# Kernel optimization log

Measured on AMD Instinct MI355X. Metric: run time of the kernel, lower is better.

The kernel has to match this reference:

```python
import jax, jax.numpy as jnp
import numpy as np

B, S, H, K = 8, 2048, 768, 128
FILTERS = (1, 3, 5)
C = H // len(FILTERS)  # 256 channels per conv, concat -> H
LN_EPS = 1e-05
COS_EPS = 1e-08


def setup_inputs() -> dict:
    key = jax.random.key(0)
    ks = jax.random.split(key, 16)
    mk = lambda k, shape: jax.random.normal(k, shape, dtype=jnp.float32) * 0.02
    return {
        "representation": jax.random.normal(ks[0], (B, S, H), dtype=jnp.float32),
        "src_mask": jnp.ones((B, S), dtype=jnp.float32),
        # conv weights stored as [k, H_in, C_out] for lax 1D conv (torch Conv2d(1,C,(k,H)))
        "enc_conv_w1": mk(ks[1], (1, H, C)),
        "enc_conv_w3": mk(ks[2], (3, H, C)),
        "enc_conv_w5": mk(ks[3], (5, H, C)),
        "ln_g": jnp.ones((H,), jnp.float32),
        "ln_b": jnp.zeros((H,), jnp.float32),
        "enc_lin_w": mk(ks[4], (H, H)),   # torch Linear weight [out,in]
        "enc_tr_w": mk(ks[5], (K, H)),
        "dec_tr_w": mk(ks[6], (H, K)),
        "dec_conv_w1": mk(ks[7], (1, H, C)),
        "dec_conv_w3": mk(ks[8], (3, H, C)),
        "dec_conv_w5": mk(ks[9], (5, H, C)),
        "dec_lin_w": mk(ks[10], (H, H)),
        "out_lin_w": mk(ks[11], (H, H)),
    }


def _multi_conv(x, ws):
    # x: [B, S, H]; each w: [k, H, C]; torch pads (k//2, 0) -> same-length for odd k
    outs = []
    for w in ws:
        k = w.shape[0]
        outs.append(jax.lax.conv_general_dilated(
            x, w, window_strides=(1,), padding=[(k // 2, k // 2)],
            dimension_numbers=("NWC", "WIO", "NWC")))
    return jnp.concatenate(outs, axis=-1)  # [B, S, H]


def _layernorm(x, g, b):
    mu = jnp.mean(x, axis=-1, keepdims=True)
    var = jnp.mean((x - mu) ** 2, axis=-1, keepdims=True)
    return (x - mu) * jax.lax.rsqrt(var + LN_EPS) * g + b


def reference(representation, src_mask, enc_conv_w1, enc_conv_w3, enc_conv_w5,
              ln_g, ln_b, enc_lin_w, enc_tr_w, dec_tr_w,
              dec_conv_w1, dec_conv_w3, dec_conv_w5, dec_lin_w, out_lin_w):
    # ---- AutoEncoder (dropout layers are identity in eval mode) ----
    h = _multi_conv(representation, (enc_conv_w1, enc_conv_w3, enc_conv_w5))
    h = _layernorm(h + representation, ln_g, ln_b)
    h = jnp.tanh(h @ enc_lin_w.T)
    location = h @ enc_tr_w.T            # [B, S, K] (encode_out)
    d = location @ dec_tr_w.T            # [B, S, H]
    d = _multi_conv(d, (dec_conv_w1, dec_conv_w3, dec_conv_w5))
    d = jnp.tanh(d @ dec_lin_w.T)
    decode_out = d @ out_lin_w.T         # [B, S, H]

    # ---- banded pairwise cosine similarity (fuses the torch shift loop) ----
    # torch loop writes dis_matrix[b, i, i+s+1] = cos(loc[b, i+s+1], loc[b, i])
    # for s in range(max_act_len), i.e. the strict upper band of the symmetric
    # pairwise cosine-similarity matrix with offsets 1..max_act_len.
    normed = location / jnp.maximum(
        jnp.sqrt(jnp.sum(location * location, axis=-1, keepdims=True)), COS_EPS)
    sim = jnp.einsum("bid,bjd->bij", normed, normed)  # [B, S, S]
    offs = jnp.arange(S)[None, :] - jnp.arange(S)[:, None]  # j - i
    max_act_len = jnp.max(jnp.sum(src_mask, axis=-1)).astype(jnp.int32)
    band = (offs >= 1) & (offs <= max_act_len)        # [S, S]
    dis_matrix = jnp.where(band[None], sim, 0.0)
    src_dis_mask = src_mask[:, :, None] * src_mask[:, None, :]
    act_dis_tags = band[None].astype(jnp.float32) * src_dis_mask
    return (location, dis_matrix, act_dis_tags, decode_out)
```

## Files before the change

### kernel.cpp

```cpp
#include <hip/hip_runtime.h>

#define B_   8
#define S_   2048
#define H_   768
#define K_   128
#define C_   256
#define SH_  2052
#define MTOK (B_*S_)

typedef __attribute__((ext_vector_type(8))) short short8;
typedef __attribute__((ext_vector_type(4))) float f32x4;

typedef __attribute__((address_space(1))) const void gvoid;
typedef __attribute__((address_space(3))) void lvoid;

__device__ __forceinline__ void gload16(const void* g, void* l) {
    __builtin_amdgcn_global_load_lds((gvoid*)g, (lvoid*)l, 16, 0, 0);
}

__device__ __forceinline__ ushort f2b(float f) {
    union { float f; unsigned u; } v; v.f = f;
    unsigned r = v.u + 0x7fffu + ((v.u >> 16) & 1u);
    return (ushort)(r >> 16);
}
__device__ __forceinline__ float b2f(ushort u) {
    union { unsigned u; float f; } v; v.u = ((unsigned)u) << 16;
    return v.f;
}
__device__ __forceinline__ float fast_tanh(float x) {
    float e = __expf(2.f * x);
    return 1.f - 2.f / (e + 1.f);
}


__global__ __launch_bounds__(512) void k_maxlen(const float* __restrict__ mask, int* Lp) {
    __shared__ float sh[8];
    const int tid = threadIdx.x;
    float mx = 0.f;
    for (int b = 0; b < B_; ++b) {
        const float4 v = ((const float4*)(mask + b * S_))[tid];
        float s = v.x + v.y + v.z + v.w;
#pragma unroll
        for (int off = 32; off; off >>= 1) s += __shfl_xor(s, off);
        if ((tid & 63) == 0) sh[tid >> 6] = s;
        __syncthreads();
        if (tid == 0) {
            float t = 0.f;
#pragma unroll
            for (int q = 0; q < 8; ++q) t += sh[q];
            mx = fmaxf(mx, t);
        }
        __syncthreads();
    }
    if (tid == 0) *Lp = (int)mx;
}

__global__ void k_build_xh(const float* __restrict__ rep, ushort* __restrict__ xh) {
    int i = blockIdx.x * blockDim.x + threadIdx.x;
    const int stride = gridDim.x * blockDim.x;
    const int n4 = B_ * SH_ * H_ / 4;
    for (; i < n4; i += stride) {
        const int idx = i * 4;
        const int h = idx % H_;
        const int rs = idx / H_;
        const int s = rs % SH_;
        const int b = rs / SH_;
        ushort4 o; o.x = 0; o.y = 0; o.z = 0; o.w = 0;
        if (s >= 2 && s < S_ + 2) {
            const float4 v = *(const float4*)(rep + ((size_t)b * S_ + (s - 2)) * H_ + h);
            o.x = f2b(v.x); o.y = f2b(v.y); o.z = f2b(v.z); o.w = f2b(v.w);
        }
        *(ushort4*)(xh + idx) = o;
    }
}

struct CvtE { const float* src; ushort* dst; int n; int kh; };
struct CvtAll { CvtE e[11]; };

__global__ void k_cvt_all(CvtAll a) {
    const CvtE e = a.e[blockIdx.y];
    int i = blockIdx.x * blockDim.x + threadIdx.x;
    const int stride = gridDim.x * blockDim.x;
    for (; i < e.n; i += stride) {
        if (e.kh) {
            const int c = i / e.kh;
            const int r = i - c * e.kh;
            e.dst[i] = f2b(e.src[r * C_ + c]);
        } else {
            e.dst[i] = f2b(e.src[i]);
        }
    }
}


struct G3P {
    const ushort* A;
    const ushort* W0;
    const ushort* W1;
    const ushort* W2;
    int Ktot;
    int lda;
    ushort* outB; int ldoB;
    float*  outF; int ldoF;
    int act;
    int nMtiles;
};

template<bool CONV>
__global__ __launch_bounds__(512, 2) void g3(G3P p) {
    constexpr int ASEG = 1024;
    constexpr int BSEG = 2048;
    constexpr int BUFE = (ASEG + BSEG) * 8;
    __shared__ __align__(16) ushort lds[3][BUFE];

    const int tid = threadIdx.x;
    const int w = tid >> 6, lane = tid & 63;
    const int l15 = lane & 15, lk = lane >> 4;
    const int wr = w >> 2, wc = w & 3;
    const int axor = l15 & 7;

    int m_base, n_base, nt, Ktot, arow0;
    const ushort* Wt;
    if (CONV) {
        const int nM = p.nMtiles;
        int idx = blockIdx.x;
        int br;
        if (idx < nM) br = 2;
        else if (idx < 2 * nM) { br = 1; idx -= nM; }
        else { br = 0; idx -= 2 * nM; }
        m_base = idx * 128;
        n_base = br * 256;
        nt = 12 * (2 * br + 1);
        Ktot = 768 * (2 * br + 1);
        Wt = (br == 0) ? p.W0 : (br == 1) ? p.W1 : p.W2;
        arow0 = m_base + ((m_base >> 11) << 2) + (2 - br);
    } else {
        m_base = blockIdx.x * 128;
        n_base = blockIdx.y * 256;
        nt = p.Ktot >> 6;
        Ktot = p.Ktot;
        Wt = p.W0;
        arow0 = m_base;
    }

    auto stage1 = [&](int kt, int bufi, int q) {
        const int kk = kt << 6;
        int rowoff = 0, h0 = kk;
        if (CONV) { const int tap = kt / 12; rowoff = tap; h0 = (kt - tap * 12) << 6; }
        if (q < 2) {
            const int seg = q * 512 + tid;
            const int row = seg >> 3;
            const int slot = (seg & 7) ^ (row & 7);
            gload16(p.A + (size_t)(arow0 + rowoff + row) * p.lda + h0 + slot * 8,
                    &lds[bufi][seg * 8]);
        } else {
            const int seg = (q - 2) * 512 + tid;
            const int row = seg >> 3;
            const int slot = (seg & 7) ^ (row & 7);
            const int wrow = (CONV ? 0 : n_base) + row;
            gload16(Wt + (size_t)wrow * Ktot + kk + slot * 8,
                    &lds[bufi][ASEG * 8 + seg * 8]);
        }
    };
    auto stage = [&](int kt, int bufi) {
#pragma unroll
        for (int q = 0; q < 6; ++q) stage1(kt, bufi, q);
    };

    f32x4 acc[4][4] = {};

    stage(0, 0);
    stage(1, 1);

    int buf = 0;
    for (int t = 0; t < nt; ++t) {
        const ushort* Ab = &lds[buf][0];
        const ushort* Bb = &lds[buf][ASEG * 8];
        if (t + 1 < nt) asm volatile("s_waitcnt vmcnt(6)" ::: "memory");
        else            asm volatile("s_waitcnt vmcnt(0)" ::: "memory");
        __builtin_amdgcn_sched_barrier(0);
        asm volatile("s_barrier" ::: "memory");
        __builtin_amdgcn_sched_barrier(0);

        int nbuf = buf + 2; if (nbuf >= 3) nbuf -= 3;
        const bool sb = (t + 2 < nt);

#pragma unroll
        for (int ks = 0; ks < 2; ++ks) {
            short8 bq[4], aq[4];
#pragma unroll
            for (int ni = 0; ni < 4; ++ni)
                bq[ni] = *(const short8*)(Bb + (wc * 64 + ni * 16 + l15) * 64 + ((((ks << 2) | lk) ^ axor) << 3));
#pragma unroll
            for (int mi = 0; mi < 4; ++mi)
                aq[mi] = *(const short8*)(Ab + (wr * 64 + mi * 16 + l15) * 64 + ((((ks << 2) | lk) ^ axor) << 3));
            if (sb) { stage1(t + 2, nbuf, 3 * ks); stage1(t + 2, nbuf, 3 * ks + 1); stage1(t + 2, nbuf, 3 * ks + 2); }
            asm volatile("s_waitcnt lgkmcnt(0)" ::: "memory");
            __builtin_amdgcn_sched_barrier(0);
            __builtin_amdgcn_s_setprio(1);
#pragma unroll
            for (int mi = 0; mi < 4; ++mi)
#pragma unroll
                for (int ni = 0; ni < 4; ++ni)
                    acc[mi][ni] = __builtin_amdgcn_mfma_f32_16x16x32_bf16(aq[mi], bq[ni], acc[mi][ni], 0, 0, 0);
            __builtin_amdgcn_s_setprio(0);
            __builtin_amdgcn_sched_barrier(0);
        }
        ++buf; if (buf == 3) buf = 0;
    }

#pragma unroll
    for (int mi = 0; mi < 4; ++mi)
#pragma unroll
        for (int ni = 0; ni < 4; ++ni)
#pragma unroll
            for (int jj = 0; jj < 4; ++jj) {
                const int r = m_base + wr * 64 + mi * 16 + 4 * lk + jj;
                const int n = n_base + wc * 64 + ni * 16 + l15;
                float v = acc[mi][ni][jj];
                if (p.act) v = fast_tanh(v);
                if (p.outF) p.outF[(size_t)r * p.ldoF + n] = v;
                if (p.outB) p.outB[(size_t)r * p.ldoB + n] = f2b(v);
            }
}


struct GemmP {
    const ushort* A;
    const ushort* Wt;
    int Ktot;
    int lda;
    ushort* outB;
    int ldoB;
    int outB_halo;
    float* outF;
    int ldoF;
    int act;
};

template<int BM, int BN>
__global__ __launch_bounds__(256) void gemm_lds(GemmP p) {
    constexpr int MF = BM / 32;
    constexpr int NF = BN / 32;
    __shared__ __align__(16) ushort As[BM * 64];
    __shared__ __align__(16) ushort Bs[BN * 64];
    const int tid = threadIdx.x;
    const int w = tid >> 6, lane = tid & 63;
    const int l15 = lane & 15, lk = lane >> 4;
    const int m_base = blockIdx.x * BM;
    const int n_base = blockIdx.y * BN;
    const int wr = w >> 1, wc = w & 1;
    f32x4 acc[MF][NF] = {};
    const int srow = lane >> 3;
    const int scol = (lane & 7) * 8;
    const int nk = p.Ktot >> 6;

    for (int kt = 0; kt < nk; ++kt) {
        const int kk = kt << 6;
#pragma unroll
        for (int q = 0; q < BM / 32; ++q) {
            const int r = w * (BM / 4) + q * 8;
            gload16(p.A + (size_t)(m_base + r + srow) * p.lda + kk + scol, As + r * 64);
        }
#pragma unroll
        for (int q = 0; q < BN / 32; ++q) {
            const int r = w * (BN / 4) + q * 8;
            gload16(p.Wt + (size_t)(n_base + r + srow) * p.Ktot + kk + scol, Bs + r * 64);
        }
        __syncthreads();
#pragma unroll
        for (int ks = 0; ks < 2; ++ks) {
            short8 af[MF], bfr[NF];
#pragma unroll
            for (int i = 0; i < MF; ++i)
                af[i] = *(const short8*)(As + (wr * (BM / 2) + i * 16 + l15) * 64 + ks * 32 + 8 * lk);
#pragma unroll
            for (int j = 0; j < NF; ++j)
                bfr[j] = *(const short8*)(Bs + (wc * (BN / 2) + j * 16 + l15) * 64 + ks * 32 + 8 * lk);
#pragma unroll
            for (int i = 0; i < MF; ++i)
#pragma unroll
                for (int j = 0; j < NF; ++j)
                    acc[i][j] = __builtin_amdgcn_mfma_f32_16x16x32_bf16(af[i], bfr[j], acc[i][j], 0, 0, 0);
        }
        __syncthreads();
    }

    const int bb4 = ((m_base >> 11) << 2) + 2;
#pragma unroll
    for (int i = 0; i < MF; ++i)
#pragma unroll
        for (int j = 0; j < NF; ++j)
#pragma unroll
            for (int jj = 0; jj < 4; ++jj) {
                const int r = m_base + wr * (BM / 2) + i * 16 + 4 * lk + jj;
                const int n = n_base + wc * (BN / 2) + j * 16 + l15;
                float v = acc[i][j][jj];
                if (p.act) v = fast_tanh(v);
                if (p.outF) p.outF[(size_t)r * p.ldoF + n] = v;
                if (p.outB) {
                    const int rr = p.outB_halo ? (r + bb4) : r;
                    p.outB[(size_t)rr * p.ldoB + n] = f2b(v);
                }
            }
}


__global__ __launch_bounds__(192) void k_ln(const ushort* __restrict__ conv,
                                            const float* __restrict__ rep,
                                            const float* __restrict__ gw,
                                            const float* __restrict__ bw,
                                            ushort* __restrict__ out) {
    const int row = blockIdx.x;
    const int tid = threadIdx.x;
    const int h = tid * 4;
    const ushort4 cv = *(const ushort4*)(conv + (size_t)row * H_ + h);
    const float4  rv = *(const float4*)(rep + (size_t)row * H_ + h);
    float v[4] = { b2f(cv.x) + rv.x, b2f(cv.y) + rv.y, b2f(cv.z) + rv.z, b2f(cv.w) + rv.w };
    float s1 = v[0] + v[1] + v[2] + v[3];
    float s2 = v[0]*v[0] + v[1]*v[1] + v[2]*v[2] + v[3]*v[3];
#pragma unroll
    for (int off = 32; off; off >>= 1) { s1 += __shfl_xor(s1, off); s2 += __shfl_xor(s2, off); }
    __shared__ float sh[6];
    const int wid = tid >> 6, lane = tid & 63;
    if (lane == 0) { sh[wid] = s1; sh[3 + wid] = s2; }
    __syncthreads();
    s1 = sh[0] + sh[1] + sh[2];
    s2 = sh[3] + sh[4] + sh[5];
    const float mu  = s1 * (1.f / H_);
    const float var = s2 * (1.f / H_) - mu * mu;
    const float rs  = rsqrtf(var + 1e-5f);
    const float4 gv = *(const float4*)(gw + h);
    const float4 bv = *(const float4*)(bw + h);
    ushort4 o;
    o.x = f2b((v[0] - mu) * rs * gv.x + bv.x);
    o.y = f2b((v[1] - mu) * rs * gv.y + bv.y);
    o.z = f2b((v[2] - mu) * rs * gv.z + bv.z);
    o.w = f2b((v[3] - mu) * rs * gv.w + bv.w);
    *(ushort4*)(out + (size_t)row * H_ + h) = o;
}


__global__ __launch_bounds__(256) void k_normed(const float* __restrict__ loc, ushort* __restrict__ out) {
    const int wid = threadIdx.x >> 6, lane = threadIdx.x & 63;
    const int row = blockIdx.x * 4 + wid;
    const float* lp = loc + (size_t)row * K_;
    const float x0 = lp[lane], x1 = lp[lane + 64];
    float ss = x0 * x0 + x1 * x1;
#pragma unroll
    for (int off = 32; off; off >>= 1) ss += __shfl_xor(ss, off);
    const float sc = 1.f / fmaxf(sqrtf(ss), 1e-8f);
    ushort* op = out + (size_t)row * K_;
    op[lane] = f2b(x0 * sc);
    op[lane + 64] = f2b(x1 * sc);
}


__global__ __launch_bounds__(256) void k_simtags(const ushort* __restrict__ normed,
                                                 const float* __restrict__ mask,
                                                 const int* __restrict__ Lp,
                                                 float* __restrict__ dis,
                                                 float* __restrict__ tags) {
    const int wid = threadIdx.x >> 6, lane = threadIdx.x & 63;
    const int l15 = lane & 15, lk = lane >> 4;
    const int b   = blockIdx.z;
    const int i0b = blockIdx.x * 64;
    const int i0  = i0b + wid * 16;
    const int j0  = blockIdx.y * 64;
    const int L   = *Lp;
    f32x4 acc[4] = {};
    if ((j0 + 63 >= i0b + 1) && (j0 <= i0b + 63 + L)) {
        const ushort* nb = normed + (size_t)b * S_ * K_;
#pragma unroll
        for (int kt = 0; kt < 4; ++kt) {
            const int kk = kt * 32;
            const short8 a = *(const short8*)(nb + (size_t)(i0 + l15) * K_ + kk + 8 * lk);
#pragma unroll
            for (int j = 0; j < 4; ++j) {
                const short8 bfr = *(const short8*)(nb + (size_t)(j0 + j * 16 + l15) * K_ + kk + 8 * lk);
                acc[j] = __builtin_amdgcn_mfma_f32_16x16x32_bf16(a, bfr, acc[j], 0, 0, 0);
            }
        }
    }
    const float* mb = mask + b * S_;
    float* dp = dis  + (size_t)b * S_ * S_;
    float* tp = tags + (size_t)b * S_ * S_;
#pragma unroll
    for (int j = 0; j < 4; ++j) {
#pragma unroll
        for (int jj = 0; jj < 4; ++jj) {
            const int i  = i0 + 4 * lk + jj;
            const int jc = j0 + j * 16 + l15;
            const int d  = jc - i;
            const bool band = (d >= 1 && d <= L);
            dp[(size_t)i * S_ + jc] = band ? acc[j][jj] : 0.f;
            tp[(size_t)i * S_ + jc] = band ? mb[i] * mb[jc] : 0.f;
        }
    }
}


extern "C" void kernel_launch(void* const* d_in, const int* in_sizes, int n_in,
                              void* d_out, int out_size, void* d_ws, size_t ws_size,
                              hipStream_t stream) {
    const float* rep  = (const float*)d_in[0];
    const float* mask = (const float*)d_in[1];
    const float* ew1  = (const float*)d_in[2];
    const float* ew3  = (const float*)d_in[3];
    const float* ew5  = (const float*)d_in[4];
    const float* lng  = (const float*)d_in[5];
    const float* lnb  = (const float*)d_in[6];
    const float* elin = (const float*)d_in[7];
    const float* etr  = (const float*)d_in[8];
    const float* dtr  = (const float*)d_in[9];
    const float* dw1  = (const float*)d_in[10];
    const float* dw3  = (const float*)d_in[11];
    const float* dw5  = (const float*)d_in[12];
    const float* dlin = (const float*)d_in[13];
    const float* olin = (const float*)d_in[14];

    float* out_loc = (float*)d_out;
    float* out_dis = out_loc + (size_t)B_ * S_ * K_;
    float* out_tag = out_dis + (size_t)B_ * S_ * S_;
    float* out_dec = out_tag + (size_t)B_ * S_ * S_;

    char* ws = (char*)d_ws;
    size_t off = 0;
    auto alloc = [&](size_t bytes) -> char* {
        char* p = ws + off;
        off += (bytes + 255) & ~(size_t)255;
        return p;
    };
    int*    Lp    = (int*)alloc(256);
    ushort* Xh    = (ushort*)alloc((size_t)B_ * SH_ * H_ * 2);
    ushort* wte1  = (ushort*)alloc((size_t)C_ * 768 * 2);
    ushort* wte3  = (ushort*)alloc((size_t)C_ * 2304 * 2);
    ushort* wte5  = (ushort*)alloc((size_t)C_ * 3840 * 2);
    ushort* wtd1  = (ushort*)alloc((size_t)C_ * 768 * 2);
    ushort* wtd3  = (ushort*)alloc((size_t)C_ * 2304 * 2);
    ushort* wtd5  = (ushort*)alloc((size_t)C_ * 3840 * 2);
    ushort* welin = (ushort*)alloc((size_t)H_ * H_ * 2);
    ushort* wetr  = (ushort*)alloc((size_t)K_ * H_ * 2);
    ushort* wdtr  = (ushort*)alloc((size_t)H_ * K_ * 2);
    ushort* wdlin = (ushort*)alloc((size_t)H_ * H_ * 2);
    ushort* wolin = (ushort*)alloc((size_t)H_ * H_ * 2);
    ushort* bufB  = (ushort*)alloc((size_t)MTOK * H_ * 2);
    ushort* bufC  = (ushort*)alloc((size_t)MTOK * H_ * 2);
    ushort* bufD  = (ushort*)alloc((size_t)MTOK * H_ * 2);
    ushort* bufL  = (ushort*)alloc((size_t)MTOK * K_ * 2);
    ushort* bufN  = (ushort*)alloc((size_t)MTOK * K_ * 2);
    if (ws_size < off) return;

    k_maxlen<<<1, 512, 0, stream>>>(mask, Lp);
    k_build_xh<<<2048, 256, 0, stream>>>(rep, Xh);

    CvtAll ca;
    ca.e[0]  = { ew1,  wte1, 768 * C_,  768 };
    ca.e[1]  = { ew3,  wte3, 2304 * C_, 2304 };
    ca.e[2]  = { ew5,  wte5, 3840 * C_, 3840 };
    ca.e[3]  = { dw1,  wtd1, 768 * C_,  768 };
    ca.e[4]  = { dw3,  wtd3, 2304 * C_, 2304 };
    ca.e[5]  = { dw5,  wtd5, 3840 * C_, 3840 };
    ca.e[6]  = { elin, welin, H_ * H_, 0 };
    ca.e[7]  = { etr,  wetr,  K_ * H_, 0 };
    ca.e[8]  = { dtr,  wdtr,  H_ * K_, 0 };
    ca.e[9]  = { dlin, wdlin, H_ * H_, 0 };
    ca.e[10] = { olin, wolin, H_ * H_, 0 };
    k_cvt_all<<<dim3(256, 11), 256, 0, stream>>>(ca);

    {
        G3P p{}; p.A = Xh; p.W0 = wte1; p.W1 = wte3; p.W2 = wte5;
        p.lda = H_; p.outB = bufB; p.ldoB = H_; p.nMtiles = MTOK / 128;
        g3<true><<<3 * (MTOK / 128), 512, 0, stream>>>(p);
    }
    k_ln<<<MTOK, 192, 0, stream>>>(bufB, rep, lng, lnb, bufC);
    {
        G3P p{}; p.A = bufC; p.W0 = welin; p.Ktot = H_; p.lda = H_;
        p.outB = bufD; p.ldoB = H_; p.act = 1;
        g3<false><<<dim3(MTOK / 128, H_ / 256), 512, 0, stream>>>(p);
    }
    {
        GemmP p{}; p.A = bufD; p.lda = H_; p.Wt = wetr; p.Ktot = H_;
        p.outF = out_loc; p.ldoF = K_; p.outB = bufL; p.ldoB = K_;
        gemm_lds<64, 128><<<dim3(MTOK / 64, 1), 256, 0, stream>>>(p);
    }
    k_normed<<<MTOK / 4, 256, 0, stream>>>(out_loc, bufN);
    {
        GemmP p{}; p.A = bufL; p.lda = K_; p.Wt = wdtr; p.Ktot = K_;
        p.outB = Xh; p.ldoB = H_; p.outB_halo = 1;
        gemm_lds<128, 128><<<dim3(MTOK / 128, H_ / 128), 256, 0, stream>>>(p);
    }
    {
        G3P p{}; p.A = Xh; p.W0 = wtd1; p.W1 = wtd3; p.W2 = wtd5;
        p.lda = H_; p.outB = bufB; p.ldoB = H_; p.nMtiles = MTOK / 128;
        g3<true><<<3 * (MTOK / 128), 512, 0, stream>>>(p);
    }
    {
        G3P p{}; p.A = bufB; p.W0 = wdlin; p.Ktot = H_; p.lda = H_;
        p.outB = bufC; p.ldoB = H_; p.act = 1;
        g3<false><<<dim3(MTOK / 128, H_ / 256), 512, 0, stream>>>(p);
    }
    {
        G3P p{}; p.A = bufC; p.W0 = wolin; p.Ktot = H_; p.lda = H_;
        p.outF = out_dec; p.ldoF = H_;
        g3<false><<<dim3(MTOK / 128, H_ / 256), 512, 0, stream>>>(p);
    }
    k_simtags<<<dim3(S_ / 64, S_ / 64, B_), 256, 0, stream>>>(bufN, mask, Lp, out_dis, out_tag);
}
```

Baseline: 447.7 us.

## Use 256x256 tiles and split-K the 5-tap conv for balanced blocks

Replaces the 128x256 triple-buffered GEMM with a 256x256 double-buffered kernel that loads the A fragments in two halves, which raises reuse per LDS load. The conv grid is reorganised into four equal-work sets of 256 blocks by splitting the 5-tap branch's K into two partial sums held in fp32. The LayerNorm, or a new merge kernel on the decoder side, adds those partials. This aims to balance conv block durations and cut global traffic per FLOP, at the cost of extra fp32 partial-buffer traffic, one more kernel launch, and lower occupancy from larger tiles.

Measured after the change: 486.8 us. +8.7%, slower.

```diff
diff --git a/kernel.cpp b/kernel.cpp
--- a/kernel.cpp
+++ b/kernel.cpp
@@ -93,25 +93,22 @@
 }
 
 
-struct G3P {
+struct GBP {
     const ushort* A;
-    const ushort* W0;
-    const ushort* W1;
-    const ushort* W2;
+    const ushort* W;
+    const ushort* w1; const ushort* w3; const ushort* w5;
     int Ktot;
     int lda;
     ushort* outB; int ldoB;
     float*  outF; int ldoF;
     int act;
-    int nMtiles;
+    ushort* convB;
+    float* PA; float* PB;
 };
 
 template<bool CONV>
-__global__ __launch_bounds__(512, 2) void g3(G3P p) {
-    constexpr int ASEG = 1024;
-    constexpr int BSEG = 2048;
-    constexpr int BUFE = (ASEG + BSEG) * 8;
-    __shared__ __align__(16) ushort lds[3][BUFE];
+__global__ __launch_bounds__(512) void gemm_big(GBP p) {
+    __shared__ __align__(16) ushort lds[2][4096 * 8];
 
     const int tid = threadIdx.x;
     const int w = tid >> 6, lane = tid & 63;
@@ -119,108 +116,127 @@
     const int wr = w >> 2, wc = w & 3;
     const int axor = l15 & 7;
 
-    int m_base, n_base, nt, Ktot, arow0;
+    int m_base, n_base = 0, nt, kbase = 0, abase = 0, set = 0, wstride, lda = p.lda;
     const ushort* Wt;
     if (CONV) {
-        const int nM = p.nMtiles;
-        int idx = blockIdx.x;
-        int br;
-        if (idx < nM) br = 2;
-        else if (idx < 2 * nM) { br = 1; idx -= nM; }
-        else { br = 0; idx -= 2 * nM; }
-        m_base = idx * 128;
-        n_base = br * 256;
-        nt = 12 * (2 * br + 1);
-        Ktot = 768 * (2 * br + 1);
-        Wt = (br == 0) ? p.W0 : (br == 1) ? p.W1 : p.W2;
-        arow0 = m_base + ((m_base >> 11) << 2) + (2 - br);
+        set = blockIdx.x >> 6;
+        m_base = (blockIdx.x & 63) * 256;
+        if (set == 0)      { Wt = p.w5; wstride = 3840; kbase = 0;    abase = 0; nt = 36; }
+        else if (set == 1) { Wt = p.w3; wstride = 2304; kbase = 0;    abase = 1; nt = 36; }
+        else if (set == 2) { Wt = p.w5; wstride = 3840; kbase = 2304; abase = 3; nt = 24; }
+        else               { Wt = p.w1; wstride = 768;  kbase = 0;    abase = 2; nt = 12; }
     } else {
-        m_base = blockIdx.x * 128;
+        m_base = blockIdx.x * 256;
         n_base = blockIdx.y * 256;
-        nt = p.Ktot >> 6;
-        Ktot = p.Ktot;
-        Wt = p.W0;
-        arow0 = m_base;
-    }
-
-    auto stage1 = [&](int kt, int bufi, int q) {
-        const int kk = kt << 6;
-        int rowoff = 0, h0 = kk;
-        if (CONV) { const int tap = kt / 12; rowoff = tap; h0 = (kt - tap * 12) << 6; }
-        if (q < 2) {
+        Wt = p.W; wstride = p.Ktot; nt = p.Ktot >> 6;
+    }
+    const int bb = m_base >> 11;
+    const int arow0 = CONV ? (m_base + 4 * bb + abase) : m_base;
+
+    auto stage = [&](int kt, int bufi) {
+        int klocal = kt, taprow = 0;
+        if (CONV) { taprow = kt / 12; klocal = kt - taprow * 12; }
+        const int h0 = klocal << 6;
+        const int wcol = kbase + (kt << 6);
+        ushort* Ab = &lds[bufi][0];
+        ushort* Bb = &lds[bufi][2048 * 8];
+#pragma unroll
+        for (int q = 0; q < 4; ++q) {
             const int seg = q * 512 + tid;
             const int row = seg >> 3;
-            const int slot = (seg & 7) ^ (row & 7);
-            gload16(p.A + (size_t)(arow0 + rowoff + row) * p.lda + h0 + slot * 8,
-                    &lds[bufi][seg * 8]);
-        } else {
-            const int seg = (q - 2) * 512 + tid;
+            const int s = (seg & 7) ^ (row & 7);
+            gload16(p.A + (size_t)(arow0 + taprow + row) * lda + h0 + s * 8, Ab + seg * 8);
+        }
+#pragma unroll
+        for (int q = 0; q < 4; ++q) {
+            const int seg = q * 512 + tid;
             const int row = seg >> 3;
-            const int slot = (seg & 7) ^ (row & 7);
+            const int s = (seg & 7) ^ (row & 7);
             const int wrow = (CONV ? 0 : n_base) + row;
-            gload16(Wt + (size_t)wrow * Ktot + kk + slot * 8,
-                    &lds[bufi][ASEG * 8 + seg * 8]);
+            gload16(Wt + (size_t)wrow * wstride + wcol + s * 8, Bb + seg * 8);
         }
     };
-    auto stage = [&](int kt, int bufi) {
-#pragma unroll
-        for (int q = 0; q < 6; ++q) stage1(kt, bufi, q);
-    };
-
-    f32x4 acc[4][4] = {};
+
+    f32x4 acc[8][4] = {};
 
     stage(0, 0);
     stage(1, 1);
 
-    int buf = 0;
     for (int t = 0; t < nt; ++t) {
-        const ushort* Ab = &lds[buf][0];
-        const ushort* Bb = &lds[buf][ASEG * 8];
-        if (t + 1 < nt) asm volatile("s_waitcnt vmcnt(6)" ::: "memory");
+        const int cur = t & 1;
+        const ushort* Ab = &lds[cur][0];
+        const ushort* Bb = &lds[cur][2048 * 8];
+        if (t + 1 < nt) asm volatile("s_waitcnt vmcnt(8)" ::: "memory");
         else            asm volatile("s_waitcnt vmcnt(0)" ::: "memory");
         __builtin_amdgcn_sched_barrier(0);
         asm volatile("s_barrier" ::: "memory");
         __builtin_amdgcn_sched_barrier(0);
 
-        int nbuf = buf + 2; if (nbuf >= 3) nbuf -= 3;
-        const bool sb = (t + 2 < nt);
-
-#pragma unroll
-        for (int ks = 0; ks < 2; ++ks) {
-            short8 bq[4], aq[4];
-#pragma unroll
-            for (int ni = 0; ni < 4; ++ni)
-                bq[ni] = *(const short8*)(Bb + (wc * 64 + ni * 16 + l15) * 64 + ((((ks << 2) | lk) ^ axor) << 3));
-#pragma unroll
-            for (int mi = 0; mi < 4; ++mi)
-                aq[mi] = *(const short8*)(Ab + (wr * 64 + mi * 16 + l15) * 64 + ((((ks << 2) | lk) ^ axor) << 3));
-            if (sb) { stage1(t + 2, nbuf, 3 * ks); stage1(t + 2, nbuf, 3 * ks + 1); stage1(t + 2, nbuf, 3 * ks + 2); }
-            asm volatile("s_waitcnt lgkmcnt(0)" ::: "memory");
-            __builtin_amdgcn_sched_barrier(0);
-            __builtin_amdgcn_s_setprio(1);
-#pragma unroll
-            for (int mi = 0; mi < 4; ++mi)
-#pragma unroll
-                for (int ni = 0; ni < 4; ++ni)
-                    acc[mi][ni] = __builtin_amdgcn_mfma_f32_16x16x32_bf16(aq[mi], bq[ni], acc[mi][ni], 0, 0, 0);
-            __builtin_amdgcn_s_setprio(0);
-            __builtin_amdgcn_sched_barrier(0);
-        }
-        ++buf; if (buf == 3) buf = 0;
-    }
-
-#pragma unroll
-    for (int mi = 0; mi < 4; ++mi)
+        short8 af[4][2], bf[4][2];
+#pragma unroll
+        for (int mi = 0; mi < 4; ++mi)
+#pragma unroll
+            for (int ks = 0; ks < 2; ++ks)
+                af[mi][ks] = *(const short8*)(Ab + (wr * 128 + mi * 16 + l15) * 64 + ((((ks << 2) | lk) ^ axor) << 3));
 #pragma unroll
         for (int ni = 0; ni < 4; ++ni)
 #pragma unroll
+            for (int ks = 0; ks < 2; ++ks)
+                bf[ni][ks] = *(const short8*)(Bb + (wc * 64 + ni * 16 + l15) * 64 + ((((ks << 2) | lk) ^ axor) << 3));
+        asm volatile("s_waitcnt lgkmcnt(0)" ::: "memory");
+        __builtin_amdgcn_sched_barrier(0);
+        __builtin_amdgcn_s_setprio(1);
+#pragma unroll
+        for (int mi = 0; mi < 4; ++mi)
+#pragma unroll
+            for (int ni = 0; ni < 4; ++ni) {
+                acc[mi][ni] = __builtin_amdgcn_mfma_f32_16x16x32_bf16(af[mi][0], bf[ni][0], acc[mi][ni], 0, 0, 0);
+                acc[mi][ni] = __builtin_amdgcn_mfma_f32_16x16x32_bf16(af[mi][1], bf[ni][1], acc[mi][ni], 0, 0, 0);
+            }
+        __builtin_amdgcn_s_setprio(0);
+        __builtin_amdgcn_sched_barrier(0);
+#pragma unroll
+        for (int mi = 0; mi < 4; ++mi)
+#pragma unroll
+            for (int ks = 0; ks < 2; ++ks)
+                af[mi][ks] = *(const short8*)(Ab + (wr * 128 + (4 + mi) * 16 + l15) * 64 + ((((ks << 2) | lk) ^ axor) << 3));
+        asm volatile("s_waitcnt lgkmcnt(0)" ::: "memory");
+        __builtin_amdgcn_sched_barrier(0);
+        asm volatile("s_barrier" ::: "memory");
+        __builtin_amdgcn_sched_barrier(0);
+        if (t + 2 < nt) stage(t + 2, cur);
+        __builtin_amdgcn_sched_barrier(0);
+        __builtin_amdgcn_s_setprio(1);
+#pragma unroll
+        for (int mi = 0; mi < 4; ++mi)
+#pragma unroll
+            for (int ni = 0; ni < 4; ++ni) {
+                acc[4 + mi][ni] = __builtin_amdgcn_mfma_f32_16x16x32_bf16(af[mi][0], bf[ni][0], acc[4 + mi][ni], 0, 0, 0);
+                acc[4 + mi][ni] = __builtin_amdgcn_mfma_f32_16x16x32_bf16(af[mi][1], bf[ni][1], acc[4 + mi][ni], 0, 0, 0);
+            }
+        __builtin_amdgcn_s_setprio(0);
+        __builtin_amdgcn_sched_barrier(0);
+    }
+
+#pragma unroll
+    for (int fi = 0; fi < 8; ++fi)
+#pragma unroll
+        for (int ni = 0; ni < 4; ++ni)
+#pragma unroll
             for (int jj = 0; jj < 4; ++jj) {
-                const int r = m_base + wr * 64 + mi * 16 + 4 * lk + jj;
-                const int n = n_base + wc * 64 + ni * 16 + l15;
-                float v = acc[mi][ni][jj];
-                if (p.act) v = fast_tanh(v);
-                if (p.outF) p.outF[(size_t)r * p.ldoF + n] = v;
-                if (p.outB) p.outB[(size_t)r * p.ldoB + n] = f2b(v);
+                const int r = m_base + wr * 128 + fi * 16 + 4 * lk + jj;
+                const int c = wc * 64 + ni * 16 + l15;
+                float v = acc[fi][ni][jj];
+                if (!CONV) {
+                    if (p.act) v = fast_tanh(v);
+                    if (p.outF) p.outF[(size_t)r * p.ldoF + n_base + c] = v;
+                    if (p.outB) p.outB[(size_t)r * p.ldoB + n_base + c] = f2b(v);
+                } else {
+                    if (set == 0)      p.PA[(size_t)r * 256 + c] = v;
+                    else if (set == 2) p.PB[(size_t)r * 256 + c] = v;
+                    else if (set == 1) p.convB[(size_t)r * H_ + 256 + c] = f2b(v);
+                    else               p.convB[(size_t)r * H_ + c] = f2b(v);
+                }
             }
 }
 
@@ -307,6 +323,8 @@
 
 
 __global__ __launch_bounds__(192) void k_ln(const ushort* __restrict__ conv,
+                                            const float* __restrict__ PA,
+                                            const float* __restrict__ PB,
                                             const float* __restrict__ rep,
                                             const float* __restrict__ gw,
                                             const float* __restrict__ bw,
@@ -314,9 +332,18 @@
     const int row = blockIdx.x;
     const int tid = threadIdx.x;
     const int h = tid * 4;
-    const ushort4 cv = *(const ushort4*)(conv + (size_t)row * H_ + h);
-    const float4  rv = *(const float4*)(rep + (size_t)row * H_ + h);
-    float v[4] = { b2f(cv.x) + rv.x, b2f(cv.y) + rv.y, b2f(cv.z) + rv.z, b2f(cv.w) + rv.w };
+    const float4 rv = *(const float4*)(rep + (size_t)row * H_ + h);
+    float v[4];
+    if (h < 512) {
+        const ushort4 cv = *(const ushort4*)(conv + (size_t)row * H_ + h);
+        v[0] = b2f(cv.x) + rv.x; v[1] = b2f(cv.y) + rv.y;
+        v[2] = b2f(cv.z) + rv.z; v[3] = b2f(cv.w) + rv.w;
+    } else {
+        const float4 a = *(const float4*)(PA + (size_t)row * 256 + (h - 512));
+        const float4 b = *(const float4*)(PB + (size_t)row * 256 + (h - 512));
+        v[0] = a.x + b.x + rv.x; v[1] = a.y + b.y + rv.y;
+        v[2] = a.z + b.z + rv.z; v[3] = a.w + b.w + rv.w;
+    }
     float s1 = v[0] + v[1] + v[2] + v[3];
     float s2 = v[0]*v[0] + v[1]*v[1] + v[2]*v[2] + v[3]*v[3];
 #pragma unroll
@@ -338,6 +365,25 @@
     o.z = f2b((v[2] - mu) * rs * gv.z + bv.z);
     o.w = f2b((v[3] - mu) * rs * gv.w + bv.w);
     *(ushort4*)(out + (size_t)row * H_ + h) = o;
+}
+
+
+__global__ void k_merge(const float* __restrict__ PA, const float* __restrict__ PB,
+                        ushort* __restrict__ out) {
+    int i = blockIdx.x * blockDim.x + threadIdx.x;
+    const int stride = gridDim.x * blockDim.x;
+    const int n4 = MTOK * 256 / 4;
+    for (; i < n4; i += stride) {
+        const int idx = i * 4;
+        const int row = idx >> 8;
+        const int c = idx & 255;
+        const float4 a = *(const float4*)(PA + idx);
+        const float4 b = *(const float4*)(PB + idx);
+        ushort4 o;
+        o.x = f2b(a.x + b.x); o.y = f2b(a.y + b.y);
+        o.z = f2b(a.z + b.z); o.w = f2b(a.w + b.w);
+        *(ushort4*)(out + (size_t)row * H_ + 512 + c) = o;
+    }
 }
 
 
@@ -449,6 +495,8 @@
     ushort* bufD  = (ushort*)alloc((size_t)MTOK * H_ * 2);
     ushort* bufL  = (ushort*)alloc((size_t)MTOK * K_ * 2);
     ushort* bufN  = (ushort*)alloc((size_t)MTOK * K_ * 2);
+    float*  PB    = (float*)alloc((size_t)MTOK * 256 * 4);
+    float*  PA    = (float*)bufD;
     if (ws_size < off) return;
 
     k_maxlen<<<1, 512, 0, stream>>>(mask, Lp);
@@ -469,15 +517,15 @@
     k_cvt_all<<<dim3(256, 11), 256, 0, stream>>>(ca);
 
     {
-        G3P p{}; p.A = Xh; p.W0 = wte1; p.W1 = wte3; p.W2 = wte5;
-        p.lda = H_; p.outB = bufB; p.ldoB = H_; p.nMtiles = MTOK / 128;
-        g3<true><<<3 * (MTOK / 128), 512, 0, stream>>>(p);
-    }
-    k_ln<<<MTOK, 192, 0, stream>>>(bufB, rep, lng, lnb, bufC);
-    {
-        G3P p{}; p.A = bufC; p.W0 = welin; p.Ktot = H_; p.lda = H_;
+        GBP p{}; p.A = Xh; p.w1 = wte1; p.w3 = wte3; p.w5 = wte5;
+        p.lda = H_; p.convB = bufB; p.PA = PA; p.PB = PB;
+        gemm_big<true><<<256, 512, 0, stream>>>(p);
+    }
+    k_ln<<<MTOK, 192, 0, stream>>>(bufB, PA, PB, rep, lng, lnb, bufC);
+    {
+        GBP p{}; p.A = bufC; p.W = welin; p.Ktot = H_; p.lda = H_;
         p.outB = bufD; p.ldoB = H_; p.act = 1;
-        g3<false><<<dim3(MTOK / 128, H_ / 256), 512, 0, stream>>>(p);
+        gemm_big<false><<<dim3(MTOK / 256, H_ / 256), 512, 0, stream>>>(p);
     }
     {
         GemmP p{}; p.A = bufD; p.lda = H_; p.Wt = wetr; p.Ktot = H_;
@@ -491,19 +539,20 @@
         gemm_lds<128, 128><<<dim3(MTOK / 128, H_ / 128), 256, 0, stream>>>(p);
     }
     {
-        G3P p{}; p.A = Xh; p.W0 = wtd1; p.W1 = wtd3; p.W2 = wtd5;
-        p.lda = H_; p.outB = bufB; p.ldoB = H_; p.nMtiles = MTOK / 128;
-        g3<true><<<3 * (MTOK / 128), 512, 0, stream>>>(p);
-    }
-    {
-        G3P p{}; p.A = bufB; p.W0 = wdlin; p.Ktot = H_; p.lda = H_;
+        GBP p{}; p.A = Xh; p.w1 = wtd1; p.w3 = wtd3; p.w5 = wtd5;
+        p.lda = H_; p.convB = bufB; p.PA = PA; p.PB = PB;
+        gemm_big<true><<<256, 512, 0, stream>>>(p);
+    }
+    k_merge<<<2048, 256, 0, stream>>>(PA, PB, bufB);
+    {
+        GBP p{}; p.A = bufB; p.W = wdlin; p.Ktot = H_; p.lda = H_;
         p.outB = bufC; p.ldoB = H_; p.act = 1;
-        g3<false><<<dim3(MTOK / 128, H_ / 256), 512, 0, stream>>>(p);
-    }
-    {
-        G3P p{}; p.A = bufC; p.W0 = wolin; p.Ktot = H_; p.lda = H_;
+        gemm_big<false><<<dim3(MTOK / 256, H_ / 256), 512, 0, stream>>>(p);
+    }
+    {
+        GBP p{}; p.A = bufC; p.W = wolin; p.Ktot = H_; p.lda = H_;
         p.outF = out_dec; p.ldoF = H_;
-        g3<false><<<dim3(MTOK / 128, H_ / 256), 512, 0, stream>>>(p);
+        gemm_big<false><<<dim3(MTOK / 256, H_ / 256), 512, 0, stream>>>(p);
     }
     k_simtags<<<dim3(S_ / 64, S_ / 64, B_), 256, 0, stream>>>(bufN, mask, Lp, out_dis, out_tag);
 }
```

## Add dedicated 128x192 double-buffered GEMM kernel for the 768x768 linear layers

Applied to the files above, without the earlier changes.

Splits the shared g3 template: the conv path becomes a non-templated kernel with a bf16-only epilogue, and a new g4 kernel handles the three 768x768 linear GEMMs. g4 uses 256 threads, a 128x192 output tile, 2-stage double buffering and loads both k-substeps per stage before issuing 48 MFMAs. The grid changes from 128x3 to 128x4 blocks, which is meant to improve CU fill and the ratio of MFMA work to loads. In exchange it uses less LDS buffering depth, holds more accumulator registers per thread and has smaller workgroups.

Measured after the change: 429.2 us. 1.04x faster.

```diff
diff --git a/kernel.cpp b/kernel.cpp
--- a/kernel.cpp
+++ b/kernel.cpp
@@ -98,15 +98,11 @@
     const ushort* W0;
     const ushort* W1;
     const ushort* W2;
-    int Ktot;
     int lda;
     ushort* outB; int ldoB;
-    float*  outF; int ldoF;
-    int act;
     int nMtiles;
 };
 
-template<bool CONV>
 __global__ __launch_bounds__(512, 2) void g3(G3P p) {
     constexpr int ASEG = 1024;
     constexpr int BSEG = 2048;
@@ -119,46 +115,34 @@
     const int wr = w >> 2, wc = w & 3;
     const int axor = l15 & 7;
 
-    int m_base, n_base, nt, Ktot, arow0;
-    const ushort* Wt;
-    if (CONV) {
-        const int nM = p.nMtiles;
-        int idx = blockIdx.x;
-        int br;
-        if (idx < nM) br = 2;
-        else if (idx < 2 * nM) { br = 1; idx -= nM; }
-        else { br = 0; idx -= 2 * nM; }
-        m_base = idx * 128;
-        n_base = br * 256;
-        nt = 12 * (2 * br + 1);
-        Ktot = 768 * (2 * br + 1);
-        Wt = (br == 0) ? p.W0 : (br == 1) ? p.W1 : p.W2;
-        arow0 = m_base + ((m_base >> 11) << 2) + (2 - br);
-    } else {
-        m_base = blockIdx.x * 128;
-        n_base = blockIdx.y * 256;
-        nt = p.Ktot >> 6;
-        Ktot = p.Ktot;
-        Wt = p.W0;
-        arow0 = m_base;
-    }
+    const int nM = p.nMtiles;
+    int idx = blockIdx.x;
+    int br;
+    if (idx < nM) br = 2;
+    else if (idx < 2 * nM) { br = 1; idx -= nM; }
+    else { br = 0; idx -= 2 * nM; }
+    const int m_base = idx * 128;
+    const int n_base = br * 256;
+    const int nt = 12 * (2 * br + 1);
+    const int Ktot = 768 * (2 * br + 1);
+    const ushort* Wt = (br == 0) ? p.W0 : (br == 1) ? p.W1 : p.W2;
+    const int arow0 = m_base + ((m_base >> 11) << 2) + (2 - br);
 
     auto stage1 = [&](int kt, int bufi, int q) {
         const int kk = kt << 6;
-        int rowoff = 0, h0 = kk;
-        if (CONV) { const int tap = kt / 12; rowoff = tap; h0 = (kt - tap * 12) << 6; }
+        const int tap = kt / 12;
+        const int h0 = (kt - tap * 12) << 6;
         if (q < 2) {
             const int seg = q * 512 + tid;
             const int row = seg >> 3;
             const int slot = (seg & 7) ^ (row & 7);
-            gload16(p.A + (size_t)(arow0 + rowoff + row) * p.lda + h0 + slot * 8,
+            gload16(p.A + (size_t)(arow0 + tap + row) * p.lda + h0 + slot * 8,
                     &lds[bufi][seg * 8]);
         } else {
             const int seg = (q - 2) * 512 + tid;
             const int row = seg >> 3;
             const int slot = (seg & 7) ^ (row & 7);
-            const int wrow = (CONV ? 0 : n_base) + row;
-            gload16(Wt + (size_t)wrow * Ktot + kk + slot * 8,
+            gload16(Wt + (size_t)row * Ktot + kk + slot * 8,
                     &lds[bufi][ASEG * 8 + seg * 8]);
         }
     };
@@ -217,6 +201,107 @@
             for (int jj = 0; jj < 4; ++jj) {
                 const int r = m_base + wr * 64 + mi * 16 + 4 * lk + jj;
                 const int n = n_base + wc * 64 + ni * 16 + l15;
+                p.outB[(size_t)r * p.ldoB + n] = f2b(acc[mi][ni][jj]);
+            }
+}
+
+
+struct G4P {
+    const ushort* A;
+    const ushort* W;
+    int Ktot;
+    int lda;
+    ushort* outB; int ldoB;
+    float*  outF; int ldoF;
+    int act;
+};
+
+__global__ __launch_bounds__(256, 2) void g4(G4P p) {
+    constexpr int ASEG = 1024;
+    constexpr int BSEG = 1536;
+    __shared__ __align__(16) ushort lds[2][(ASEG + BSEG) * 8];
+
+    const int tid = threadIdx.x;
+    const int w = tid >> 6, lane = tid & 63;
+    const int l15 = lane & 15, lk = lane >> 4;
+    const int wr = w >> 1, wc = w & 1;
+    const int axor = l15 & 7;
+    const int m_base = blockIdx.x * 128;
+    const int n_base = blockIdx.y * 192;
+    const int nt = p.Ktot >> 6;
+
+    auto stage = [&](int kt, int bufi) {
+        const int kk = kt << 6;
+        ushort* Ab = &lds[bufi][0];
+        ushort* Bb = &lds[bufi][ASEG * 8];
+#pragma unroll
+        for (int q = 0; q < 4; ++q) {
+            const int seg = q * 256 + tid;
+            const int row = seg >> 3;
+            const int s = (seg & 7) ^ (row & 7);
+            gload16(p.A + (size_t)(m_base + row) * p.lda + kk + s * 8, Ab + seg * 8);
+        }
+#pragma unroll
+        for (int q = 0; q < 6; ++q) {
+            const int seg = q * 256 + tid;
+            const int row = seg >> 3;
+            const int s = (seg & 7) ^ (row & 7);
+            gload16(p.W + (size_t)(n_base + row) * p.Ktot + kk + s * 8, Bb + seg * 8);
+        }
+    };
+
+    f32x4 acc[4][6] = {};
+
+    stage(0, 0);
+    stage(1, 1);
+
+    for (int t = 0; t < nt; ++t) {
+        const int cur = t & 1;
+        const ushort* Ab = &lds[cur][0];
+        const ushort* Bb = &lds[cur][ASEG * 8];
+        if (t + 1 < nt) asm volatile("s_waitcnt vmcnt(10)" ::: "memory");
+        else            asm volatile("s_waitcnt vmcnt(0)" ::: "memory");
+        __builtin_amdgcn_sched_barrier(0);
+        asm volatile("s_barrier" ::: "memory");
+        __builtin_amdgcn_sched_barrier(0);
+
+        short8 af[4][2], bf[6][2];
+#pragma unroll
+        for (int mi = 0; mi < 4; ++mi)
+#pragma unroll
+            for (int ks = 0; ks < 2; ++ks)
+                af[mi][ks] = *(const short8*)(Ab + (wr * 64 + mi * 16 + l15) * 64 + ((((ks << 2) | lk) ^ axor) << 3));
+#pragma unroll
+        for (int ni = 0; ni < 6; ++ni)
+#pragma unroll
+            for (int ks = 0; ks < 2; ++ks)
+                bf[ni][ks] = *(const short8*)(Bb + (wc * 96 + ni * 16 + l15) * 64 + ((((ks << 2) | lk) ^ axor) << 3));
+        asm volatile("s_waitcnt lgkmcnt(0)" ::: "memory");
+        __builtin_amdgcn_sched_barrier(0);
+        asm volatile("s_barrier" ::: "memory");
+        __builtin_amdgcn_sched_barrier(0);
+        if (t + 2 < nt) stage(t + 2, cur);
+        __builtin_amdgcn_sched_barrier(0);
+        __builtin_amdgcn_s_setprio(1);
+#pragma unroll
+        for (int mi = 0; mi < 4; ++mi)
+#pragma unroll
+            for (int ni = 0; ni < 6; ++ni) {
+                acc[mi][ni] = __builtin_amdgcn_mfma_f32_16x16x32_bf16(af[mi][0], bf[ni][0], acc[mi][ni], 0, 0, 0);
+                acc[mi][ni] = __builtin_amdgcn_mfma_f32_16x16x32_bf16(af[mi][1], bf[ni][1], acc[mi][ni], 0, 0, 0);
+            }
+        __builtin_amdgcn_s_setprio(0);
+        __builtin_amdgcn_sched_barrier(0);
+    }
+
+#pragma unroll
+    for (int mi = 0; mi < 4; ++mi)
+#pragma unroll
+        for (int ni = 0; ni < 6; ++ni)
+#pragma unroll
+            for (int jj = 0; jj < 4; ++jj) {
+                const int r = m_base + wr * 64 + mi * 16 + 4 * lk + jj;
+                const int n = n_base + wc * 96 + ni * 16 + l15;
                 float v = acc[mi][ni][jj];
                 if (p.act) v = fast_tanh(v);
                 if (p.outF) p.outF[(size_t)r * p.ldoF + n] = v;
@@ -471,13 +556,13 @@
     {
         G3P p{}; p.A = Xh; p.W0 = wte1; p.W1 = wte3; p.W2 = wte5;
         p.lda = H_; p.outB = bufB; p.ldoB = H_; p.nMtiles = MTOK / 128;
-        g3<true><<<3 * (MTOK / 128), 512, 0, stream>>>(p);
+        g3<<<3 * (MTOK / 128), 512, 0, stream>>>(p);
     }
     k_ln<<<MTOK, 192, 0, stream>>>(bufB, rep, lng, lnb, bufC);
     {
-        G3P p{}; p.A = bufC; p.W0 = welin; p.Ktot = H_; p.lda = H_;
+        G4P p{}; p.A = bufC; p.W = welin; p.Ktot = H_; p.lda = H_;
         p.outB = bufD; p.ldoB = H_; p.act = 1;
-        g3<false><<<dim3(MTOK / 128, H_ / 256), 512, 0, stream>>>(p);
+        g4<<<dim3(MTOK / 128, H_ / 192), 256, 0, stream>>>(p);
     }
     {
         GemmP p{}; p.A = bufD; p.lda = H_; p.Wt = wetr; p.Ktot = H_;
@@ -493,17 +578,17 @@
     {
         G3P p{}; p.A = Xh; p.W0 = wtd1; p.W1 = wtd3; p.W2 = wtd5;
         p.lda = H_; p.outB = bufB; p.ldoB = H_; p.nMtiles = MTOK / 128;
-        g3<true><<<3 * (MTOK / 128), 512, 0, stream>>>(p);
-    }
-    {
-        G3P p{}; p.A = bufB; p.W0 = wdlin; p.Ktot = H_; p.lda = H_;
+        g3<<<3 * (MTOK / 128), 512, 0, stream>>>(p);
+    }
+    {
+        G4P p{}; p.A = bufB; p.W = wdlin; p.Ktot = H_; p.lda = H_;
         p.outB = bufC; p.ldoB = H_; p.act = 1;
-        g3<false><<<dim3(MTOK / 128, H_ / 256), 512, 0, stream>>>(p);
-    }
-    {
-        G3P p{}; p.A = bufC; p.W0 = wolin; p.Ktot = H_; p.lda = H_;
+        g4<<<dim3(MTOK / 128, H_ / 192), 256, 0, stream>>>(p);
+    }
+    {
+        G4P p{}; p.A = bufC; p.W = wolin; p.Ktot = H_; p.lda = H_;
         p.outF = out_dec; p.ldoF = H_;
-        g3<false><<<dim3(MTOK / 128, H_ / 256), 512, 0, stream>>>(p);
+        g4<<<dim3(MTOK / 128, H_ / 192), 256, 0, stream>>>(p);
     }
     k_simtags<<<dim3(S_ / 64, S_ / 64, B_), 256, 0, stream>>>(bufN, mask, Lp, out_dis, out_tag);
 }
```
